# Kernel tuning notes

Hardware: AMD Instinct MI355X
Metric: run time of the kernel (lower is better)

The kernel has to match this reference:

```python
import jax, jax.numpy as jnp
import numpy as np

D_HIDN = 64
SCALE = 1.0 / np.sqrt(D_HIDN).astype(np.float32)
MASK_FILL = -1e9


def setup_inputs() -> dict:
    key = jax.random.key(0)
    kq, kk, kv, km = jax.random.split(key, 4)
    B, H, S, D = 4, 16, 2048, 64
    Q = jax.random.normal(kq, (B, H, S, D), dtype=jnp.float32)
    K = jax.random.normal(kk, (B, H, S, D), dtype=jnp.float32)
    V = jax.random.normal(kv, (B, H, S, D), dtype=jnp.float32)
    attn_mask = jax.random.randint(km, (B, H, S, S), 0, 2).astype(jnp.bool_)
    return {"Q": Q, "K": K, "V": V, "attn_mask": attn_mask}


def reference(Q, K, V, attn_mask):
    # scores = Q K^T * scale  -> [B,H,S,S]
    scores = jnp.einsum("bhqd,bhkd->bhqk", Q, K) * SCALE
    scores = jnp.where(attn_mask, MASK_FILL, scores)
    attn_prob = jax.nn.softmax(scores, axis=-1)
    # dropout is identity in eval / deterministic reference
    context = jnp.einsum("bhqk,bhkd->bhqd", attn_prob, V)
    return (context, attn_prob)
```

## Files before the change

### kernel.cpp

```cpp
#include <hip/hip_runtime.h>
#include <stdint.h>

#define SEQ 2048
#define DIM 64
#define QBLK 16
#define NWAVE 8
#define KPW 256
#define NCT 16
#define NCHUNK 8
#define THREADS 512
#define SCALE 0.125f
#define LOG2E 1.4426950408889634f
#define PSTR 40
#define VPAD 18
#define NTSTR (32*VPAD + 8)

typedef __attribute__((ext_vector_type(4))) float f32x4;
typedef __attribute__((ext_vector_type(4))) int   i32x4;
typedef __attribute__((ext_vector_type(8))) __bf16 bf16x8;

static __device__ __forceinline__ unsigned bfbits(float x) {
    union { __bf16 b; unsigned short u; } cv; cv.b = (__bf16)x; return (unsigned)cv.u;
}
static __device__ __forceinline__ float lo16(unsigned u) { return __uint_as_float(u << 16); }
static __device__ __forceinline__ float hi16(unsigned u) { return __uint_as_float(u & 0xffff0000u); }
static __device__ __forceinline__ bf16x8 cvt8(f32x4 a, f32x4 b) {
    bf16x8 f;
    f[0]=(__bf16)a[0]; f[1]=(__bf16)a[1]; f[2]=(__bf16)a[2]; f[3]=(__bf16)a[3];
    f[4]=(__bf16)b[0]; f[5]=(__bf16)b[1]; f[6]=(__bf16)b[2]; f[7]=(__bf16)b[3];
    return f;
}
static __device__ __forceinline__ unsigned nib4(i32x4 mm) {
    return (mm[0]?1u:0u) | (mm[1]?2u:0u) | (mm[2]?4u:0u) | (mm[3]?8u:0u);
}

struct WaveBuf {
    union {
        __bf16 vbuf[4 * NTSTR];
        float  ctx[QBLK * DIM];
    };
};
struct SharedT {
    WaveBuf sw[NWAVE];
    __bf16 plds[NWAVE][QBLK][PSTR];
    float red_m[QBLK][NWAVE];
    float red_s[QBLK][NWAVE];
};

__global__ __launch_bounds__(THREADS, 4)
void sdpa_mfma13(const float* __restrict__ Q, const float* __restrict__ K,
                 const float* __restrict__ V, const int* __restrict__ mask,
                 float* __restrict__ ctx_out, float* __restrict__ prob_out) {
    __shared__ SharedT su;

    const int rb   = ((blockIdx.x & 7) << 10) + (blockIdx.x >> 3);
    const int bh   = rb >> 7;
    const int q0   = (rb & 127) * QBLK;
    const int t    = threadIdx.x;
    const int lane = t & 63;
    const int w    = t >> 6;
    const int g    = lane >> 4;
    const int c    = lane & 15;

    const size_t bh_off = (size_t)bh * SEQ * DIM;
    const float* Qb = Q + bh_off;
    const float* Kb = K + bh_off;
    const float* Vb = V + bh_off;
    const int*   Mb = mask + (size_t)bh * SEQ * SEQ;
    const int wbase = w * KPW;

    bf16x8 qf[2];
    {
        const float* qr = Qb + (size_t)(q0 + c) * DIM + 8 * g;
        qf[0] = cvt8(*(const f32x4*)(qr),      *(const f32x4*)(qr + 4));
        qf[1] = cvt8(*(const f32x4*)(qr + 32), *(const f32x4*)(qr + 36));
    }

    unsigned sc_pk[2 * NCT];
    unsigned mbits0 = 0u, mbits1 = 0u;
    const int* mrow = Mb + (size_t)(q0 + c) * SEQ + wbase + 4 * g;
    f32x4 kr[4];
    i32x4 mq[8];

    #pragma unroll
    for (int j = 0; j < 8; ++j) mq[j] = *(const i32x4*)(mrow + 16 * j);
    __builtin_amdgcn_sched_barrier(0);
    {
        const float* k0 = Kb + (size_t)(wbase + c) * DIM + 8 * g;
        kr[0] = *(const f32x4*)(k0);      kr[1] = *(const f32x4*)(k0 + 4);
        kr[2] = *(const f32x4*)(k0 + 32); kr[3] = *(const f32x4*)(k0 + 36);
    }
    #pragma unroll
    for (int ct = 0; ct < 8; ++ct) {
        bf16x8 kf0 = cvt8(kr[0], kr[1]);
        bf16x8 kf1 = cvt8(kr[2], kr[3]);
        {
            const float* kn = Kb + (size_t)(wbase + (ct + 1) * 16 + c) * DIM + 8 * g;
            kr[0] = *(const f32x4*)(kn);      kr[1] = *(const f32x4*)(kn + 4);
            kr[2] = *(const f32x4*)(kn + 32); kr[3] = *(const f32x4*)(kn + 36);
        }
        f32x4 acc = {0.f, 0.f, 0.f, 0.f};
        acc = __builtin_amdgcn_mfma_f32_16x16x32_bf16(kf0, qf[0], acc, 0, 0, 0);
        acc = __builtin_amdgcn_mfma_f32_16x16x32_bf16(kf1, qf[1], acc, 0, 0, 0);
        sc_pk[2 * ct]     = bfbits(acc[0] * SCALE) | (bfbits(acc[1] * SCALE) << 16);
        sc_pk[2 * ct + 1] = bfbits(acc[2] * SCALE) | (bfbits(acc[3] * SCALE) << 16);
    }
    #pragma unroll
    for (int j = 0; j < 8; ++j) mbits0 |= nib4(mq[j]) << (4 * j);

    #pragma unroll
    for (int j = 0; j < 8; ++j) mq[j] = *(const i32x4*)(mrow + 16 * (8 + j));
    __builtin_amdgcn_sched_barrier(0);
    #pragma unroll
    for (int ct = 8; ct < NCT; ++ct) {
        bf16x8 kf0 = cvt8(kr[0], kr[1]);
        bf16x8 kf1 = cvt8(kr[2], kr[3]);
        if (ct + 1 < NCT) {
            const float* kn = Kb + (size_t)(wbase + (ct + 1) * 16 + c) * DIM + 8 * g;
            kr[0] = *(const f32x4*)(kn);      kr[1] = *(const f32x4*)(kn + 4);
            kr[2] = *(const f32x4*)(kn + 32); kr[3] = *(const f32x4*)(kn + 36);
        }
        f32x4 acc = {0.f, 0.f, 0.f, 0.f};
        acc = __builtin_amdgcn_mfma_f32_16x16x32_bf16(kf0, qf[0], acc, 0, 0, 0);
        acc = __builtin_amdgcn_mfma_f32_16x16x32_bf16(kf1, qf[1], acc, 0, 0, 0);
        sc_pk[2 * ct]     = bfbits(acc[0] * SCALE) | (bfbits(acc[1] * SCALE) << 16);
        sc_pk[2 * ct + 1] = bfbits(acc[2] * SCALE) | (bfbits(acc[3] * SCALE) << 16);
    }
    #pragma unroll
    for (int j = 0; j < 8; ++j) mbits1 |= nib4(mq[j]) << (4 * j);

    const int r_st = lane >> 4;
    const int cw   = (4 * c) & 15;
    const int ntw  = c >> 2;
    f32x4 vrawA[4], vrawB[4];
    {
        const float* vsrc = Vb + (size_t)(wbase + r_st) * DIM + 4 * c;
        #pragma unroll
        for (int i = 0; i < 4; ++i) {
            vrawA[i] = *(const f32x4*)(vsrc + (size_t)(4 * i) * DIM);
            vrawB[i] = *(const f32x4*)(vsrc + (size_t)(16 + 4 * i) * DIM);
        }
    }

    #pragma unroll
    for (int ct = 0; ct < NCT; ++ct) {
        unsigned nib = ((ct < 8) ? (mbits0 >> (4 * ct)) : (mbits1 >> (4 * (ct - 8)))) & 0xFu;
        float x0 = (nib & 1u) ? -1e9f : lo16(sc_pk[2 * ct]);
        float x1 = (nib & 2u) ? -1e9f : hi16(sc_pk[2 * ct]);
        float x2 = (nib & 4u) ? -1e9f : lo16(sc_pk[2 * ct + 1]);
        float x3 = (nib & 8u) ? -1e9f : hi16(sc_pk[2 * ct + 1]);
        sc_pk[2 * ct]     = bfbits(x0) | (bfbits(x1) << 16);
        sc_pk[2 * ct + 1] = bfbits(x2) | (bfbits(x3) << 16);
    }

    float mx = -3e38f;
    #pragma unroll
    for (int i = 0; i < 2 * NCT; ++i)
        mx = fmaxf(mx, fmaxf(lo16(sc_pk[i]), hi16(sc_pk[i])));
    mx = fmaxf(mx, __shfl_xor(mx, 16));
    mx = fmaxf(mx, __shfl_xor(mx, 32));
    if (g == 0) su.red_m[c][w] = mx;
    __syncthreads();
    float M = su.red_m[c][0];
    #pragma unroll
    for (int i = 1; i < NWAVE; ++i) M = fmaxf(M, su.red_m[c][i]);

    float sum = 0.f;
    #pragma unroll
    for (int i = 0; i < 2 * NCT; ++i) {
        float e0 = exp2f((lo16(sc_pk[i]) - M) * LOG2E);
        float e1 = exp2f((hi16(sc_pk[i]) - M) * LOG2E);
        sum += e0 + e1;
        sc_pk[i] = bfbits(e0) | (bfbits(e1) << 16);
    }
    sum += __shfl_xor(sum, 16);
    sum += __shfl_xor(sum, 32);
    if (g == 0) su.red_s[c][w] = sum;
    __syncthreads();
    float S = 0.f;
    #pragma unroll
    for (int i = 0; i < NWAVE; ++i) S += su.red_s[c][i];
    const float inv = 1.0f / S;
    float invr[4];
    #pragma unroll
    for (int jr = 0; jr < 4; ++jr) invr[jr] = __shfl(inv, 4 * g + jr);

    f32x4 cacc[4];
    #pragma unroll
    for (int nt = 0; nt < 4; ++nt) cacc[nt] = (f32x4){0.f, 0.f, 0.f, 0.f};

    float* prow = prob_out + ((size_t)bh * SEQ + (q0 + c)) * SEQ + wbase;
    __bf16* vbufW = su.sw[w].vbuf;

    #pragma unroll
    for (int cc = 0; cc < NCHUNK; ++cc) {
        #pragma unroll
        for (int i = 0; i < 4; ++i) {
            ushort2 lo_, hi_;
            lo_.x = (unsigned short)bfbits(vrawA[i][0]);
            lo_.y = (unsigned short)bfbits(vrawA[i][1]);
            hi_.x = (unsigned short)bfbits(vrawA[i][2]);
            hi_.y = (unsigned short)bfbits(vrawA[i][3]);
            __bf16* p = &vbufW[ntw * NTSTR + (4 * i + r_st) * VPAD + cw];
            *(ushort2*)p = lo_;
            *(ushort2*)(p + 2) = hi_;
        }
        #pragma unroll
        for (int i = 0; i < 4; ++i) {
            ushort2 lo_, hi_;
            lo_.x = (unsigned short)bfbits(vrawB[i][0]);
            lo_.y = (unsigned short)bfbits(vrawB[i][1]);
            hi_.x = (unsigned short)bfbits(vrawB[i][2]);
            hi_.y = (unsigned short)bfbits(vrawB[i][3]);
            __bf16* p = &vbufW[ntw * NTSTR + (16 + 4 * i + r_st) * VPAD + cw];
            *(ushort2*)p = lo_;
            *(ushort2*)(p + 2) = hi_;
        }
        if (cc + 1 < NCHUNK) {
            const float* vsrc = Vb + (size_t)(wbase + (cc + 1) * 32 + r_st) * DIM + 4 * c;
            #pragma unroll
            for (int i = 0; i < 4; ++i) {
                vrawA[i] = *(const f32x4*)(vsrc + (size_t)(4 * i) * DIM);
                vrawB[i] = *(const f32x4*)(vsrc + (size_t)(16 + 4 * i) * DIM);
            }
        }

        unsigned pkA0 = sc_pk[4 * cc],     pkA1 = sc_pk[4 * cc + 1];
        unsigned pkB0 = sc_pk[4 * cc + 2], pkB1 = sc_pk[4 * cc + 3];
        {
            f32x4 pnA = { lo16(pkA0) * inv, hi16(pkA0) * inv, lo16(pkA1) * inv, hi16(pkA1) * inv };
            f32x4 pnB = { lo16(pkB0) * inv, hi16(pkB0) * inv, lo16(pkB1) * inv, hi16(pkB1) * inv };
            *(f32x4*)(prow + 32 * cc + 4 * g)      = pnA;
            *(f32x4*)(prow + 32 * cc + 16 + 4 * g) = pnB;
        }
        {
            uint2 ua; ua.x = pkA0; ua.y = pkA1;
            uint2 ub; ub.x = pkB0; ub.y = pkB1;
            *(uint2*)&su.plds[w][c][4 * g]      = ua;
            *(uint2*)&su.plds[w][c][16 + 4 * g] = ub;
        }
        bf16x8 pf = *(const bf16x8*)&su.plds[w][c][8 * g];

        bf16x8 vfr[4];
        #pragma unroll
        for (int nt = 0; nt < 4; ++nt) {
            bf16x8 f;
            #pragma unroll
            for (int j = 0; j < 8; ++j)
                f[j] = vbufW[nt * NTSTR + (8 * g + j) * VPAD + c];
            vfr[nt] = f;
        }

        __builtin_amdgcn_s_setprio(1);
        #pragma unroll
        for (int nt = 0; nt < 4; ++nt)
            cacc[nt] = __builtin_amdgcn_mfma_f32_16x16x32_bf16(pf, vfr[nt], cacc[nt], 0, 0, 0);
        __builtin_amdgcn_s_setprio(0);
    }

    #pragma unroll
    for (int nt = 0; nt < 4; ++nt)
        #pragma unroll
        for (int jr = 0; jr < 4; ++jr)
            su.sw[w].ctx[(4 * g + jr) * DIM + nt * 16 + c] = cacc[nt][jr] * invr[jr];
    __syncthreads();
    {
        int e = t * 2;
        float2 a = make_float2(0.f, 0.f);
        #pragma unroll
        for (int i = 0; i < NWAVE; ++i) {
            float2 v = *(const float2*)&su.sw[i].ctx[e];
            a.x += v.x; a.y += v.y;
        }
        *(float2*)(ctx_out + ((size_t)bh * SEQ + q0) * DIM + e) = a;
    }
}

extern "C" void kernel_launch(void* const* d_in, const int* in_sizes, int n_in,
                              void* d_out, int out_size, void* d_ws, size_t ws_size,
                              hipStream_t stream) {
    const float* Q = (const float*)d_in[0];
    const float* K = (const float*)d_in[1];
    const float* V = (const float*)d_in[2];
    const int* mask = (const int*)d_in[3];
    float* ctx  = (float*)d_out;
    float* prob = (float*)d_out + (size_t)4 * 16 * SEQ * DIM;

    dim3 grid(64 * (SEQ / QBLK));
    dim3 block(THREADS);
    sdpa_mfma13<<<grid, block, 0, stream>>>(Q, K, V, mask, ctx, prob);
}
```

Baseline: 979.1 us.

## Merge softmax reductions into one barrier and build P fragments with shuffles

Each wave now computes exponentials against its own local max and publishes both the local max and sum together. A single block barrier then combines them with online-softmax rescaling, replacing the two barriers the max and sum passes needed before. The P operand for the MFMA is now gathered through cross-lane shuffles instead of an LDS store and reload, which also removes the plds shared array. Costs are extra shuffles and per-wave exp rescaling, plus a slight change in bf16 rounding because exponentials are taken relative to the local max.

New measurement: 1.001 ms. +2.2%, slower.

```diff
diff --git a/kernel.cpp b/kernel.cpp
--- a/kernel.cpp
+++ b/kernel.cpp
@@ -11,13 +11,14 @@
 #define THREADS 512
 #define SCALE 0.125f
 #define LOG2E 1.4426950408889634f
-#define PSTR 40
 #define VPAD 18
 #define NTSTR (32*VPAD + 8)
 
 typedef __attribute__((ext_vector_type(4))) float f32x4;
 typedef __attribute__((ext_vector_type(4))) int   i32x4;
 typedef __attribute__((ext_vector_type(8))) __bf16 bf16x8;
+
+union PFrag { unsigned w[4]; bf16x8 f; };
 
 static __device__ __forceinline__ unsigned bfbits(float x) {
     union { __bf16 b; unsigned short u; } cv; cv.b = (__bf16)x; return (unsigned)cv.u;
@@ -42,13 +43,12 @@
 };
 struct SharedT {
     WaveBuf sw[NWAVE];
-    __bf16 plds[NWAVE][QBLK][PSTR];
     float red_m[QBLK][NWAVE];
     float red_s[QBLK][NWAVE];
 };
 
 __global__ __launch_bounds__(THREADS, 4)
-void sdpa_mfma13(const float* __restrict__ Q, const float* __restrict__ K,
+void sdpa_mfma16(const float* __restrict__ Q, const float* __restrict__ K,
                  const float* __restrict__ V, const int* __restrict__ mask,
                  float* __restrict__ ctx_out, float* __restrict__ prob_out) {
     __shared__ SharedT su;
@@ -159,35 +159,42 @@
         mx = fmaxf(mx, fmaxf(lo16(sc_pk[i]), hi16(sc_pk[i])));
     mx = fmaxf(mx, __shfl_xor(mx, 16));
     mx = fmaxf(mx, __shfl_xor(mx, 32));
-    if (g == 0) su.red_m[c][w] = mx;
+
+    float sw_ = 0.f;
+    #pragma unroll
+    for (int i = 0; i < 2 * NCT; ++i) {
+        float e0 = exp2f((lo16(sc_pk[i]) - mx) * LOG2E);
+        float e1 = exp2f((hi16(sc_pk[i]) - mx) * LOG2E);
+        sw_ += e0 + e1;
+        sc_pk[i] = bfbits(e0) | (bfbits(e1) << 16);
+    }
+    sw_ += __shfl_xor(sw_, 16);
+    sw_ += __shfl_xor(sw_, 32);
+    if (g == 0) { su.red_m[c][w] = mx; su.red_s[c][w] = sw_; }
     __syncthreads();
-    float M = su.red_m[c][0];
-    #pragma unroll
-    for (int i = 1; i < NWAVE; ++i) M = fmaxf(M, su.red_m[c][i]);
-
-    float sum = 0.f;
-    #pragma unroll
-    for (int i = 0; i < 2 * NCT; ++i) {
-        float e0 = exp2f((lo16(sc_pk[i]) - M) * LOG2E);
-        float e1 = exp2f((hi16(sc_pk[i]) - M) * LOG2E);
-        sum += e0 + e1;
-        sc_pk[i] = bfbits(e0) | (bfbits(e1) << 16);
-    }
-    sum += __shfl_xor(sum, 16);
-    sum += __shfl_xor(sum, 32);
-    if (g == 0) su.red_s[c][w] = sum;
-    __syncthreads();
-    float S = 0.f;
-    #pragma unroll
-    for (int i = 0; i < NWAVE; ++i) S += su.red_s[c][i];
-    const float inv = 1.0f / S;
-    float invr[4];
-    #pragma unroll
-    for (int jr = 0; jr < 4; ++jr) invr[jr] = __shfl(inv, 4 * g + jr);
+
+    float fac;
+    {
+        float M = su.red_m[c][0];
+        #pragma unroll
+        for (int i = 1; i < NWAVE; ++i) M = fmaxf(M, su.red_m[c][i]);
+        float S = 0.f;
+        #pragma unroll
+        for (int i = 0; i < NWAVE; ++i)
+            S += su.red_s[c][i] * exp2f((su.red_m[c][i] - M) * LOG2E);
+        fac = exp2f((mx - M) * LOG2E) / S;
+    }
+    float facr[4];
+    #pragma unroll
+    for (int jr = 0; jr < 4; ++jr) facr[jr] = __shfl(fac, 4 * g + jr);
 
     f32x4 cacc[4];
     #pragma unroll
     for (int nt = 0; nt < 4; ++nt) cacc[nt] = (f32x4){0.f, 0.f, 0.f, 0.f};
+
+    const int  sA  = ((g & 1) << 5) + c;
+    const int  sB  = sA + 16;
+    const bool hiT = (g >> 1) != 0;
 
     float* prow = prob_out + ((size_t)bh * SEQ + (q0 + c)) * SEQ + wbase;
     __bf16* vbufW = su.sw[w].vbuf;
@@ -225,21 +232,26 @@
             }
         }
 
-        unsigned pkA0 = sc_pk[4 * cc],     pkA1 = sc_pk[4 * cc + 1];
-        unsigned pkB0 = sc_pk[4 * cc + 2], pkB1 = sc_pk[4 * cc + 3];
+        unsigned w0 = sc_pk[4 * cc],     w1 = sc_pk[4 * cc + 1];
+        unsigned w2 = sc_pk[4 * cc + 2], w3 = sc_pk[4 * cc + 3];
         {
-            f32x4 pnA = { lo16(pkA0) * inv, hi16(pkA0) * inv, lo16(pkA1) * inv, hi16(pkA1) * inv };
-            f32x4 pnB = { lo16(pkB0) * inv, hi16(pkB0) * inv, lo16(pkB1) * inv, hi16(pkB1) * inv };
+            f32x4 pnA = { lo16(w0) * fac, hi16(w0) * fac, lo16(w1) * fac, hi16(w1) * fac };
+            f32x4 pnB = { lo16(w2) * fac, hi16(w2) * fac, lo16(w3) * fac, hi16(w3) * fac };
             *(f32x4*)(prow + 32 * cc + 4 * g)      = pnA;
             *(f32x4*)(prow + 32 * cc + 16 + 4 * g) = pnB;
         }
+
+        PFrag pf;
         {
-            uint2 ua; ua.x = pkA0; ua.y = pkA1;
-            uint2 ub; ub.x = pkB0; ub.y = pkB1;
-            *(uint2*)&su.plds[w][c][4 * g]      = ua;
-            *(uint2*)&su.plds[w][c][16 + 4 * g] = ub;
-        }
-        bf16x8 pf = *(const bf16x8*)&su.plds[w][c][8 * g];
+            unsigned a0 = __shfl(w0, sA), b0 = __shfl(w2, sA);
+            pf.w[0] = hiT ? b0 : a0;
+            unsigned a1 = __shfl(w1, sA), b1 = __shfl(w3, sA);
+            pf.w[1] = hiT ? b1 : a1;
+            unsigned a2 = __shfl(w0, sB), b2 = __shfl(w2, sB);
+            pf.w[2] = hiT ? b2 : a2;
+            unsigned a3 = __shfl(w1, sB), b3 = __shfl(w3, sB);
+            pf.w[3] = hiT ? b3 : a3;
+        }
 
         bf16x8 vfr[4];
         #pragma unroll
@@ -254,7 +266,7 @@
         __builtin_amdgcn_s_setprio(1);
         #pragma unroll
         for (int nt = 0; nt < 4; ++nt)
-            cacc[nt] = __builtin_amdgcn_mfma_f32_16x16x32_bf16(pf, vfr[nt], cacc[nt], 0, 0, 0);
+            cacc[nt] = __builtin_amdgcn_mfma_f32_16x16x32_bf16(pf.f, vfr[nt], cacc[nt], 0, 0, 0);
         __builtin_amdgcn_s_setprio(0);
     }
 
@@ -262,7 +274,7 @@
     for (int nt = 0; nt < 4; ++nt)
         #pragma unroll
         for (int jr = 0; jr < 4; ++jr)
-            su.sw[w].ctx[(4 * g + jr) * DIM + nt * 16 + c] = cacc[nt][jr] * invr[jr];
+            su.sw[w].ctx[(4 * g + jr) * DIM + nt * 16 + c] = cacc[nt][jr] * facr[jr];
     __syncthreads();
     {
         int e = t * 2;
@@ -288,5 +300,5 @@
 
     dim3 grid(64 * (SEQ / QBLK));
     dim3 block(THREADS);
-    sdpa_mfma13<<<grid, block, 0, stream>>>(Q, K, V, mask, ctx, prob);
-}
+    sdpa_mfma16<<<grid, block, 0, stream>>>(Q, K, V, mask, ctx, prob);
+}
```
